# Kernel optimization log

Measured on AMD Instinct MI355X. Metric: run time of the kernel, lower is better.

## Reference

```python
import jax, jax.numpy as jnp
import numpy as np

B, N, C = 2, 2048, 768
H = 16
D = C // H  # head_dim = 48
SCALE = 1.0 / float(np.sqrt(D))


def setup_inputs() -> dict:
    key = jax.random.key(0)
    ks = jax.random.split(key, 5)
    x = jax.random.normal(ks[0], (B, N, C), dtype=jnp.float32)
    # torch nn.Linear weights are [out, in]; apply as x @ W.T
    qkv_w = jax.random.normal(ks[1], (3 * C, C), dtype=jnp.float32) * 0.02
    qkv_b = jax.random.normal(ks[2], (3 * C,), dtype=jnp.float32) * 0.02
    proj_w = jax.random.normal(ks[3], (C, C), dtype=jnp.float32) * 0.02
    proj_b = jax.random.normal(ks[4], (C,), dtype=jnp.float32) * 0.02
    return {"x": x, "qkv_w": qkv_w, "qkv_b": qkv_b, "proj_w": proj_w, "proj_b": proj_b}


def reference(x, qkv_w, qkv_b, proj_w, proj_b):
    # qkv: (B, N, 3C) -> (3, B, H, N, D)
    qkv = x @ qkv_w.T + qkv_b
    qkv = qkv.reshape(B, N, 3, H, D).transpose(2, 0, 3, 1, 4)
    q, k, v = qkv[0], qkv[1], qkv[2]
    # manual attention: full (B, H, N, N) score matrix, as in the original
    attn = jnp.einsum('bhqd,bhkd->bhqk', q, k) * SCALE
    attn = jax.nn.softmax(attn, axis=-1)
    # attn_drop with p=0.0 (eval / deterministic) is identity
    y = jnp.einsum('bhqk,bhkd->bhqd', attn, v)
    y = y.transpose(0, 2, 1, 3).reshape(B, N, C)
    return y @ proj_w.T + proj_b
```

## Files before the change

kernel.cpp:

```cpp
#include <hip/hip_runtime.h>

typedef short v8s __attribute__((ext_vector_type(8)));
typedef short v4s __attribute__((ext_vector_type(4)));
typedef float v4f __attribute__((ext_vector_type(4)));
typedef unsigned uint2v __attribute__((ext_vector_type(2)));
typedef unsigned uint4v __attribute__((ext_vector_type(4)));
typedef unsigned short u16;

#define NSEQ 2048
#define CDIM 768
#define NH   16
#define DH   48
#define DP   64
#define MROWS 4096
#define N3C  2304
#define BH   32

#if __has_builtin(__builtin_amdgcn_exp2f)
#define EXP2(x) __builtin_amdgcn_exp2f(x)
#else
#define EXP2(x) exp2f(x)
#endif
#if __has_builtin(__builtin_amdgcn_rcpf)
#define RCP(x) __builtin_amdgcn_rcpf(x)
#else
#define RCP(x) (1.0f/(x))
#endif

#if __has_builtin(__builtin_amdgcn_permlane32_swap) && __has_builtin(__builtin_amdgcn_permlane16_swap)
#define HAVE_PERMSWAP 1
#endif

__device__ __forceinline__ u16 f2bf(float f){
  unsigned u = __float_as_uint(f);
  u += 0x7FFFu + ((u>>16)&1u);
  return (u16)(u>>16);
}

#if __has_builtin(__builtin_amdgcn_cvt_pk_bf16_f32)
typedef __bf16 bf16x2_t __attribute__((ext_vector_type(2)));
__device__ __forceinline__ unsigned pkbf(float a, float b){
  bf16x2_t r = __builtin_amdgcn_cvt_pk_bf16_f32(a, b);
  return __builtin_bit_cast(unsigned, r);
}
#else
__device__ __forceinline__ unsigned pkbf(float a, float b){
  unsigned x = __float_as_uint(a), y = __float_as_uint(b);
  x += 0x7FFFu + ((x>>16)&1u);
  y += 0x7FFFu + ((y>>16)&1u);
  return (x>>16) | (y & 0xFFFF0000u);
}
#endif

__device__ __forceinline__ void load_lds16(const u16* g, u16* l){
  __builtin_amdgcn_global_load_lds((const __attribute__((address_space(1))) void*)g,
                                   (__attribute__((address_space(3))) void*)l, 16, 0, 0);
}

#define XN8  (MROWS*CDIM/8)
#define WN8  (N3C*CDIM/8)
#define PN8  (CDIM*CDIM/8)
#define CONVB ((XN8+WN8+PN8)/256)
__global__ __launch_bounds__(256) void prep(const float* __restrict__ x, const float* __restrict__ w,
                                            const float* __restrict__ pw, u16* __restrict__ dst,
                                            u16* __restrict__ q, u16* __restrict__ k){
  int bid = blockIdx.x;
  if (bid < CONVB){
    int i = bid*256 + threadIdx.x;
    const float* src;
    if (i < XN8)            src = x  + (size_t)i*8;
    else if (i < XN8+WN8)   src = w  + (size_t)(i - XN8)*8;
    else                    src = pw + (size_t)(i - XN8 - WN8)*8;
    v4f f0 = ((const v4f*)src)[0];
    v4f f1 = ((const v4f*)src)[1];
    v8s o;
#pragma unroll
    for (int j = 0; j < 4; j++) ((u16*)&o)[j]   = f2bf(f0[j]);
#pragma unroll
    for (int j = 0; j < 4; j++) ((u16*)&o)[4+j] = f2bf(f1[j]);
    ((v8s*)dst)[i] = o;
  } else {
    int idx = (bid - CONVB)*256 + threadIdx.x;
    v8s z = (v8s){0,0,0,0,0,0,0,0};
    int r = idx >> 1, half = idx & 1;
    *(v8s*)(q + (size_t)r*DP + DH + half*8) = z;
    *(v8s*)(k + (size_t)r*DP + DH + half*8) = z;
  }
}

__global__ __launch_bounds__(256) void qkv_gemm(const u16* __restrict__ x, const u16* __restrict__ w,
                                                const float* __restrict__ bias,
                                                u16* __restrict__ q, u16* __restrict__ k, u16* __restrict__ v){
  __shared__ __align__(16) u16 As[128*32];
  __shared__ __align__(16) u16 Bs[128*32];
  const int wave = threadIdx.x >> 6;
  const int lane = threadIdx.x & 63;
  const int l15  = lane & 15;
  const int quad = lane >> 4;
  const int wm = wave & 1, wn = wave >> 1;
  const int m0 = blockIdx.x*128, n0 = blockIdx.y*128;

  const int srow = lane >> 2;
  const int sg   = (lane & 3) ^ ((lane >> 3) & 3);
  const int sgoff = sg*8;

  v4f acc[4][4];
#pragma unroll
  for (int i = 0; i < 4; i++)
#pragma unroll
    for (int j = 0; j < 4; j++) acc[i][j] = (v4f){0.f,0.f,0.f,0.f};

  const int sig = (l15 >> 1) & 3;

  for (int kt = 0; kt < CDIM/32; kt++){
    const int k0 = kt*32;
    __syncthreads();
#pragma unroll
    for (int j = 0; j < 2; j++){
      int c = wave*2 + j;
      int r = c*16 + srow;
      load_lds16(x + (size_t)(m0 + r)*CDIM + k0 + sgoff, &As[c*512]);
      load_lds16(w + (size_t)(n0 + r)*CDIM + k0 + sgoff, &Bs[c*512]);
    }
    __syncthreads();

    v8s af[4], bf[4];
#pragma unroll
    for (int t = 0; t < 4; t++){
      int ra = wm*64 + t*16 + l15;
      af[t] = *(const v8s*)(&As[ra*32 + ((quad ^ sig)<<3)]);
      int rb = wn*64 + t*16 + l15;
      bf[t] = *(const v8s*)(&Bs[rb*32 + ((quad ^ sig)<<3)]);
    }
#pragma unroll
    for (int ti = 0; ti < 4; ti++)
#pragma unroll
      for (int tj = 0; tj < 4; tj++)
        acc[ti][tj] = __builtin_amdgcn_mfma_f32_16x16x32_bf16(af[ti], bf[tj], acc[ti][tj], 0, 0, 0);
  }

  const float QS = 0.2082540589f;
#pragma unroll
  for (int tj = 0; tj < 4; tj++){
    const int c = n0 + wn*64 + tj*16 + l15;
    const float bv = bias[c];
    const int t = c / CDIM;
    const int rem = c - t*CDIM;
    const int h = rem / DH;
    const int d = rem - h*DH;
#pragma unroll
    for (int ti = 0; ti < 4; ti++){
#pragma unroll
      for (int r = 0; r < 4; r++){
        int m = m0 + wm*64 + ti*16 + quad*4 + r;
        int b_ = m >> 11;
        int n  = m & (NSEQ-1);
        float val = acc[ti][tj][r] + bv;
        if (t == 0) val *= QS;
        u16 o  = f2bf(val);
        int bhn = b_*NH + h;
        if (t == 0)      q[((size_t)bhn*NSEQ + n)*DP + d] = o;
        else if (t == 1) k[((size_t)bhn*NSEQ + n)*DP + d] = o;
        else             v[((size_t)bhn*DP + d)*NSEQ + n] = o;
      }
    }
  }
}

__global__ __launch_bounds__(256, 4) void attn(const u16* __restrict__ q, const u16* __restrict__ k,
                                               const u16* __restrict__ v, u16* __restrict__ y){
  __shared__ __align__(16) u16 Kl[2][64*64];
  __shared__ __align__(16) u16 Vl[2][48*64];
#ifndef HAVE_PERMSWAP
  __shared__ __align__(16) u16 Pl[4*2*1024];
#endif
  const int bh = blockIdx.x;
  const int qt = blockIdx.y;
  const int wave = threadIdx.x >> 6;
  const int lane = threadIdx.x & 63;
  const int l15  = lane & 15;
  const int quad = lane >> 4;
  const int lo3  = l15 & 7;
  const u16* qb = q + (size_t)bh*NSEQ*DP;
  const u16* kb = k + (size_t)bh*NSEQ*DP;
  const u16* vb = v + (size_t)bh*DP*NSEQ;
  const int qm = qt*128 + wave*32;

  v8s qf[2][2];
#pragma unroll
  for (int si = 0; si < 2; si++)
#pragma unroll
    for (int ks = 0; ks < 2; ks++)
      qf[si][ks] = *(const v8s*)(qb + (size_t)(qm + si*16 + l15)*DP + ks*32 + quad*8);

  const short one = (short)0x3F80;
  const v8s vones = (l15 == 0) ? (v8s){one,one,one,one,one,one,one,one}
                               : (v8s){0,0,0,0,0,0,0,0};

  v4f o[2][4];
#pragma unroll
  for (int si = 0; si < 2; si++)
#pragma unroll
    for (int i = 0; i < 4; i++) o[si][i] = (v4f){0.f,0.f,0.f,0.f};

  const int sr  = lane >> 3;
  const int soff = ((lane & 7) ^ (sr & 7)) * 8;
#ifndef HAVE_PERMSWAP
  u16* Plw = Pl + wave*2048;
#endif

  const int krow0 = wave*8 + sr;
#define STAGE(kt_, b_) do{                                                              \
    load_lds16(kb + ((size_t)((kt_)*64 + krow0))*DP + soff,      &Kl[b_][krow0*64]);    \
    load_lds16(kb + ((size_t)((kt_)*64 + 32 + krow0))*DP + soff, &Kl[b_][(32+krow0)*64]);\
    load_lds16(vb + (size_t)krow0*NSEQ + (kt_)*64 + soff,        &Vl[b_][krow0*64]);    \
    if (wave < 2)                                                                       \
      load_lds16(vb + (size_t)(32+krow0)*NSEQ + (kt_)*64 + soff, &Vl[b_][(32+krow0)*64]);\
  } while(0)

  STAGE(0, 0);

  for (int i = 0; i < 32; i++){
    const int buf = i & 1;
    __syncthreads();
    if (i < 31) STAGE(i + 1, buf^1);

    const u16* Klb = &Kl[buf][0];
    const u16* Vlb = &Vl[buf][0];

    v4f s[2][4];
#pragma unroll
    for (int nt = 0; nt < 4; nt++){
      int rrow = nt*16 + l15;
      v8s kf0 = *(const v8s*)(&Klb[rrow*64 + ((quad ^ lo3)<<3)]);
      v8s kf1 = *(const v8s*)(&Klb[rrow*64 + (((4+quad) ^ lo3)<<3)]);
      s[0][nt] = __builtin_amdgcn_mfma_f32_16x16x32_bf16(kf0, qf[0][0], (v4f){0.f,0.f,0.f,0.f}, 0, 0, 0);
      s[0][nt] = __builtin_amdgcn_mfma_f32_16x16x32_bf16(kf1, qf[0][1], s[0][nt], 0, 0, 0);
      s[1][nt] = __builtin_amdgcn_mfma_f32_16x16x32_bf16(kf0, qf[1][0], (v4f){0.f,0.f,0.f,0.f}, 0, 0, 0);
      s[1][nt] = __builtin_amdgcn_mfma_f32_16x16x32_bf16(kf1, qf[1][1], s[1][nt], 0, 0, 0);
    }

    v8s pa[2][2];
#ifdef HAVE_PERMSWAP
#pragma unroll
    for (int si = 0; si < 2; si++){
      unsigned w[4][2];
#pragma unroll
      for (int nt = 0; nt < 4; nt++){
        w[nt][0] = pkbf(EXP2(s[si][nt][0]), EXP2(s[si][nt][1]));
        w[nt][1] = pkbf(EXP2(s[si][nt][2]), EXP2(s[si][nt][3]));
      }
#pragma unroll
      for (int ks = 0; ks < 2; ks++){
        unsigned W[4];
#pragma unroll
        for (int h = 0; h < 2; h++){
          auto a = __builtin_amdgcn_permlane32_swap(w[2*ks][h], w[2*ks+1][h], false, false);
          auto b = __builtin_amdgcn_permlane16_swap(a[0], a[1], false, false);
          W[h]   = b[0];
          W[2+h] = b[1];
        }
        uint4v u; u[0] = W[0]; u[1] = W[1]; u[2] = W[2]; u[3] = W[3];
        pa[si][ks] = __builtin_bit_cast(v8s, u);
      }
    }
#else
#pragma unroll
    for (int si = 0; si < 2; si++)
#pragma unroll
      for (int nt = 0; nt < 4; nt++){
        uint2v pw;
        pw.x = pkbf(EXP2(s[si][nt][0]), EXP2(s[si][nt][1]));
        pw.y = pkbf(EXP2(s[si][nt][2]), EXP2(s[si][nt][3]));
        int g = nt*2 + (quad>>1);
        *(uint2v*)(&Plw[si*1024 + l15*64 + ((g ^ lo3)<<3) + (quad&1)*4]) = pw;
      }
#pragma unroll
    for (int si = 0; si < 2; si++)
#pragma unroll
      for (int ks = 0; ks < 2; ks++){
        int ga = ks*4 + quad;
        pa[si][ks] = *(const v8s*)(&Plw[si*1024 + l15*64 + ((ga ^ lo3)<<3)]);
      }
#endif

#pragma unroll
    for (int dt = 0; dt < 3; dt++){
#pragma unroll
      for (int ks = 0; ks < 2; ks++){
        int row = dt*16 + l15;
        v8s vf = *(const v8s*)(&Vlb[row*64 + (((ks*4+quad) ^ lo3)<<3)]);
        o[0][dt] = __builtin_amdgcn_mfma_f32_16x16x32_bf16(pa[0][ks], vf, o[0][dt], 0, 0, 0);
        o[1][dt] = __builtin_amdgcn_mfma_f32_16x16x32_bf16(pa[1][ks], vf, o[1][dt], 0, 0, 0);
      }
    }
#pragma unroll
    for (int ks = 0; ks < 2; ks++){
      o[0][3] = __builtin_amdgcn_mfma_f32_16x16x32_bf16(pa[0][ks], vones, o[0][3], 0, 0, 0);
      o[1][3] = __builtin_amdgcn_mfma_f32_16x16x32_bf16(pa[1][ks], vones, o[1][3], 0, 0, 0);
    }
  }

  const int b_ = bh / NH, h = bh % NH;
#pragma unroll
  for (int si = 0; si < 2; si++){
#pragma unroll
    for (int r = 0; r < 4; r++){
      float l = __shfl(o[si][3][r], (lane & 48));
      float inv = RCP(l);
      int rowg = b_*NSEQ + qm + si*16 + quad*4 + r;
#pragma unroll
      for (int dt = 0; dt < 3; dt++)
        y[(size_t)rowg*CDIM + h*DH + dt*16 + l15] = f2bf(o[si][dt][r]*inv);
    }
  }
}

__global__ __launch_bounds__(256) void proj_gemm(const u16* __restrict__ y, const u16* __restrict__ w,
                                                 const float* __restrict__ bias, float* __restrict__ out){
  __shared__ __align__(16) u16 As[64*32];
  __shared__ __align__(16) u16 Bs[128*32];
  const int wave = threadIdx.x >> 6;
  const int lane = threadIdx.x & 63;
  const int l15  = lane & 15;
  const int quad = lane >> 4;
  const int wm = wave & 1, wn = wave >> 1;
  const int m0 = blockIdx.x*64, n0 = blockIdx.y*128;

  const int srow = lane >> 2;
  const int sg   = (lane & 3) ^ ((lane >> 3) & 3);
  const int sgoff = sg*8;

  v4f acc[2][4];
#pragma unroll
  for (int i = 0; i < 2; i++)
#pragma unroll
    for (int j = 0; j < 4; j++) acc[i][j] = (v4f){0.f,0.f,0.f,0.f};

  const int sig = (l15 >> 1) & 3;

  for (int kt = 0; kt < CDIM/32; kt++){
    const int k0 = kt*32;
    __syncthreads();
    {
      int rA = wave*16 + srow;
      load_lds16(y + (size_t)(m0 + rA)*CDIM + k0 + sgoff, &As[wave*512]);
#pragma unroll
      for (int j = 0; j < 2; j++){
        int c = wave*2 + j;
        int rB = c*16 + srow;
        load_lds16(w + (size_t)(n0 + rB)*CDIM + k0 + sgoff, &Bs[c*512]);
      }
    }
    __syncthreads();

    v8s af[2], bf[4];
#pragma unroll
    for (int t = 0; t < 2; t++){
      int ra = wm*32 + t*16 + l15;
      af[t] = *(const v8s*)(&As[ra*32 + ((quad ^ sig)<<3)]);
    }
#pragma unroll
    for (int t = 0; t < 4; t++){
      int rb = wn*64 + t*16 + l15;
      bf[t] = *(const v8s*)(&Bs[rb*32 + ((quad ^ sig)<<3)]);
    }
#pragma unroll
    for (int ti = 0; ti < 2; ti++)
#pragma unroll
      for (int tj = 0; tj < 4; tj++)
        acc[ti][tj] = __builtin_amdgcn_mfma_f32_16x16x32_bf16(af[ti], bf[tj], acc[ti][tj], 0, 0, 0);
  }

#pragma unroll
  for (int tj = 0; tj < 4; tj++){
    const int c = n0 + wn*64 + tj*16 + l15;
    const float bv = bias[c];
#pragma unroll
    for (int ti = 0; ti < 2; ti++){
#pragma unroll
      for (int r = 0; r < 4; r++){
        int m = m0 + wm*32 + ti*16 + quad*4 + r;
        out[(size_t)m*CDIM + c] = acc[ti][tj][r] + bv;
      }
    }
  }
}

extern "C" void kernel_launch(void* const* d_in, const int* in_sizes, int n_in,
                              void* d_out, int out_size, void* d_ws, size_t ws_size,
                              hipStream_t stream){
  const float* x      = (const float*)d_in[0];
  const float* qkv_w  = (const float*)d_in[1];
  const float* qkv_b  = (const float*)d_in[2];
  const float* proj_w = (const float*)d_in[3];
  const float* proj_b = (const float*)d_in[4];
  float* out = (float*)d_out;

  u16* xb  = (u16*)d_ws;
  u16* wb  = xb  + (size_t)MROWS*CDIM;
  u16* pwb = wb  + (size_t)N3C*CDIM;
  u16* q   = pwb + (size_t)CDIM*CDIM;
  u16* k   = q + (size_t)BH*NSEQ*DP;
  u16* v   = k + (size_t)BH*NSEQ*DP;
  u16* y = xb;

  prep<<<dim3(CONVB + 512), dim3(256), 0, stream>>>(x, qkv_w, proj_w, xb, q, k);
  qkv_gemm<<<dim3(MROWS/128, N3C/128), dim3(256), 0, stream>>>(xb, wb, qkv_b, q, k, v);
  attn<<<dim3(BH, NSEQ/128), dim3(256), 0, stream>>>(q, k, v, y);
  proj_gemm<<<dim3(MROWS/64, CDIM/128), dim3(256), 0, stream>>>(y, pwb, proj_b, out);
}
```

Measured before the change: 165.6 us.

## Triple-buffer K/V tiles in attention with explicit vmcnt waits

Moves the attention kernel's K/V LDS staging from double to triple buffering, prefetching two tiles ahead. A manual s_waitcnt vmcnt(3) plus s_barrier replaces __syncthreads so the async LDS loads for the next tile can stay in flight during compute. The goal is to hide global-load latency better. In exchange, LDS use per block rises, which may lower occupancy, and the hand-written wait count depends on how many loads each wave issues (waves 0-1 issue 4, others 3). The fallback path without permswap adds a __syncthreads inside the compute body.

```diff
diff --git a/kernel.cpp b/kernel.cpp
--- a/kernel.cpp
+++ b/kernel.cpp
@@ -169,8 +169,8 @@
 
 __global__ __launch_bounds__(256, 4) void attn(const u16* __restrict__ q, const u16* __restrict__ k,
                                                const u16* __restrict__ v, u16* __restrict__ y){
-  __shared__ __align__(16) u16 Kl[2][64*64];
-  __shared__ __align__(16) u16 Vl[2][48*64];
+  __shared__ __align__(16) u16 Kl[3][64*64];
+  __shared__ __align__(16) u16 Vl[3][48*64];
 #ifndef HAVE_PERMSWAP
   __shared__ __align__(16) u16 Pl[4*2*1024];
 #endif
@@ -186,23 +186,6 @@
   const u16* vb = v + (size_t)bh*DP*NSEQ;
   const int qm = qt*128 + wave*32;
 
-  v8s qf[2][2];
-#pragma unroll
-  for (int si = 0; si < 2; si++)
-#pragma unroll
-    for (int ks = 0; ks < 2; ks++)
-      qf[si][ks] = *(const v8s*)(qb + (size_t)(qm + si*16 + l15)*DP + ks*32 + quad*8);
-
-  const short one = (short)0x3F80;
-  const v8s vones = (l15 == 0) ? (v8s){one,one,one,one,one,one,one,one}
-                               : (v8s){0,0,0,0,0,0,0,0};
-
-  v4f o[2][4];
-#pragma unroll
-  for (int si = 0; si < 2; si++)
-#pragma unroll
-    for (int i = 0; i < 4; i++) o[si][i] = (v4f){0.f,0.f,0.f,0.f};
-
   const int sr  = lane >> 3;
   const int soff = ((lane & 7) ^ (sr & 7)) * 8;
 #ifndef HAVE_PERMSWAP
@@ -219,87 +202,114 @@
   } while(0)
 
   STAGE(0, 0);
-
-  for (int i = 0; i < 32; i++){
-    const int buf = i & 1;
-    __syncthreads();
-    if (i < 31) STAGE(i + 1, buf^1);
-
-    const u16* Klb = &Kl[buf][0];
-    const u16* Vlb = &Vl[buf][0];
-
-    v4f s[2][4];
-#pragma unroll
-    for (int nt = 0; nt < 4; nt++){
-      int rrow = nt*16 + l15;
-      v8s kf0 = *(const v8s*)(&Klb[rrow*64 + ((quad ^ lo3)<<3)]);
-      v8s kf1 = *(const v8s*)(&Klb[rrow*64 + (((4+quad) ^ lo3)<<3)]);
-      s[0][nt] = __builtin_amdgcn_mfma_f32_16x16x32_bf16(kf0, qf[0][0], (v4f){0.f,0.f,0.f,0.f}, 0, 0, 0);
-      s[0][nt] = __builtin_amdgcn_mfma_f32_16x16x32_bf16(kf1, qf[0][1], s[0][nt], 0, 0, 0);
-      s[1][nt] = __builtin_amdgcn_mfma_f32_16x16x32_bf16(kf0, qf[1][0], (v4f){0.f,0.f,0.f,0.f}, 0, 0, 0);
-      s[1][nt] = __builtin_amdgcn_mfma_f32_16x16x32_bf16(kf1, qf[1][1], s[1][nt], 0, 0, 0);
-    }
-
-    v8s pa[2][2];
+  STAGE(1, 1);
+
+  v8s qf[2][2];
+#pragma unroll
+  for (int si = 0; si < 2; si++)
+#pragma unroll
+    for (int ks = 0; ks < 2; ks++)
+      qf[si][ks] = *(const v8s*)(qb + (size_t)(qm + si*16 + l15)*DP + ks*32 + quad*8);
+
+  const short one = (short)0x3F80;
+  const v8s vones = (l15 == 0) ? (v8s){one,one,one,one,one,one,one,one}
+                               : (v8s){0,0,0,0,0,0,0,0};
+
+  v4f o[2][4];
+#pragma unroll
+  for (int si = 0; si < 2; si++)
+#pragma unroll
+    for (int i = 0; i < 4; i++) o[si][i] = (v4f){0.f,0.f,0.f,0.f};
+
+#define COMPUTE(sc_) do{                                                                          \
+    const u16* Klb = &Kl[sc_][0];                                                                 \
+    const u16* Vlb = &Vl[sc_][0];                                                                 \
+    v4f s[2][4];                                                                                  \
+    _Pragma("unroll")                                                                             \
+    for (int nt = 0; nt < 4; nt++){                                                               \
+      int rrow = nt*16 + l15;                                                                     \
+      v8s kf0 = *(const v8s*)(&Klb[rrow*64 + ((quad ^ lo3)<<3)]);                                 \
+      v8s kf1 = *(const v8s*)(&Klb[rrow*64 + (((4+quad) ^ lo3)<<3)]);                             \
+      s[0][nt] = __builtin_amdgcn_mfma_f32_16x16x32_bf16(kf0, qf[0][0], (v4f){0.f,0.f,0.f,0.f}, 0, 0, 0); \
+      s[0][nt] = __builtin_amdgcn_mfma_f32_16x16x32_bf16(kf1, qf[0][1], s[0][nt], 0, 0, 0);       \
+      s[1][nt] = __builtin_amdgcn_mfma_f32_16x16x32_bf16(kf0, qf[1][0], (v4f){0.f,0.f,0.f,0.f}, 0, 0, 0); \
+      s[1][nt] = __builtin_amdgcn_mfma_f32_16x16x32_bf16(kf1, qf[1][1], s[1][nt], 0, 0, 0);       \
+    }                                                                                             \
+    v8s pa[2][2];                                                                                 \
+    PTRANS                                                                                        \
+    _Pragma("unroll")                                                                             \
+    for (int dt = 0; dt < 3; dt++){                                                               \
+      _Pragma("unroll")                                                                           \
+      for (int ks = 0; ks < 2; ks++){                                                             \
+        int row = dt*16 + l15;                                                                    \
+        v8s vf = *(const v8s*)(&Vlb[row*64 + (((ks*4+quad) ^ lo3)<<3)]);                          \
+        o[0][dt] = __builtin_amdgcn_mfma_f32_16x16x32_bf16(pa[0][ks], vf, o[0][dt], 0, 0, 0);     \
+        o[1][dt] = __builtin_amdgcn_mfma_f32_16x16x32_bf16(pa[1][ks], vf, o[1][dt], 0, 0, 0);     \
+      }                                                                                           \
+    }                                                                                             \
+    _Pragma("unroll")                                                                             \
+    for (int ks = 0; ks < 2; ks++){                                                               \
+      o[0][3] = __builtin_amdgcn_mfma_f32_16x16x32_bf16(pa[0][ks], vones, o[0][3], 0, 0, 0);      \
+      o[1][3] = __builtin_amdgcn_mfma_f32_16x16x32_bf16(pa[1][ks], vones, o[1][3], 0, 0, 0);      \
+    }                                                                                             \
+  } while(0)
+
 #ifdef HAVE_PERMSWAP
-#pragma unroll
-    for (int si = 0; si < 2; si++){
-      unsigned w[4][2];
-#pragma unroll
-      for (int nt = 0; nt < 4; nt++){
-        w[nt][0] = pkbf(EXP2(s[si][nt][0]), EXP2(s[si][nt][1]));
-        w[nt][1] = pkbf(EXP2(s[si][nt][2]), EXP2(s[si][nt][3]));
+#define PTRANS                                                                                    \
+    _Pragma("unroll")                                                                             \
+    for (int si = 0; si < 2; si++){                                                               \
+      unsigned w[4][2];                                                                           \
+      _Pragma("unroll")                                                                           \
+      for (int nt = 0; nt < 4; nt++){                                                             \
+        w[nt][0] = pkbf(EXP2(s[si][nt][0]), EXP2(s[si][nt][1]));                                  \
+        w[nt][1] = pkbf(EXP2(s[si][nt][2]), EXP2(s[si][nt][3]));                                  \
+      }                                                                                           \
+      _Pragma("unroll")                                                                           \
+      for (int ks = 0; ks < 2; ks++){                                                             \
+        unsigned W[4];                                                                            \
+        _Pragma("unroll")                                                                         \
+        for (int h = 0; h < 2; h++){                                                              \
+          auto a = __builtin_amdgcn_permlane32_swap(w[2*ks][h], w[2*ks+1][h], false, false);      \
+          auto b = __builtin_amdgcn_permlane16_swap(a[0], a[1], false, false);                    \
+          W[h]   = b[0];                                                                          \
+          W[2+h] = b[1];                                                                          \
+        }                                                                                         \
+        uint4v u; u[0] = W[0]; u[1] = W[1]; u[2] = W[2]; u[3] = W[3];                             \
+        pa[si][ks] = __builtin_bit_cast(v8s, u);                                                  \
+      }                                                                                           \
+    }
+#else
+#define PTRANS                                                                                    \
+    _Pragma("unroll")                                                                             \
+    for (int si = 0; si < 2; si++)                                                                \
+      _Pragma("unroll")                                                                           \
+      for (int nt = 0; nt < 4; nt++){                                                             \
+        uint2v pw;                                                                                \
+        pw.x = pkbf(EXP2(s[si][nt][0]), EXP2(s[si][nt][1]));                                      \
+        pw.y = pkbf(EXP2(s[si][nt][2]), EXP2(s[si][nt][3]));                                      \
+        int g = nt*2 + (quad>>1);                                                                 \
+        *(uint2v*)(&Plw[si*1024 + l15*64 + ((g ^ lo3)<<3) + (quad&1)*4]) = pw;                    \
+      }                                                                                           \
+    __syncthreads();                                                                              \
+    _Pragma("unroll")                                                                             \
+    for (int si = 0; si < 2; si++)                                                                \
+      _Pragma("unroll")                                                                           \
+      for (int ks = 0; ks < 2; ks++){                                                             \
+        int ga = ks*4 + quad;                                                                     \
+        pa[si][ks] = *(const v8s*)(&Plw[si*1024 + l15*64 + ((ga ^ lo3)<<3)]);                     \
       }
-#pragma unroll
-      for (int ks = 0; ks < 2; ks++){
-        unsigned W[4];
-#pragma unroll
-        for (int h = 0; h < 2; h++){
-          auto a = __builtin_amdgcn_permlane32_swap(w[2*ks][h], w[2*ks+1][h], false, false);
-          auto b = __builtin_amdgcn_permlane16_swap(a[0], a[1], false, false);
-          W[h]   = b[0];
-          W[2+h] = b[1];
-        }
-        uint4v u; u[0] = W[0]; u[1] = W[1]; u[2] = W[2]; u[3] = W[3];
-        pa[si][ks] = __builtin_bit_cast(v8s, u);
-      }
-    }
-#else
-#pragma unroll
-    for (int si = 0; si < 2; si++)
-#pragma unroll
-      for (int nt = 0; nt < 4; nt++){
-        uint2v pw;
-        pw.x = pkbf(EXP2(s[si][nt][0]), EXP2(s[si][nt][1]));
-        pw.y = pkbf(EXP2(s[si][nt][2]), EXP2(s[si][nt][3]));
-        int g = nt*2 + (quad>>1);
-        *(uint2v*)(&Plw[si*1024 + l15*64 + ((g ^ lo3)<<3) + (quad&1)*4]) = pw;
-      }
-#pragma unroll
-    for (int si = 0; si < 2; si++)
-#pragma unroll
-      for (int ks = 0; ks < 2; ks++){
-        int ga = ks*4 + quad;
-        pa[si][ks] = *(const v8s*)(&Plw[si*1024 + l15*64 + ((ga ^ lo3)<<3)]);
-      }
-#endif
-
-#pragma unroll
-    for (int dt = 0; dt < 3; dt++){
-#pragma unroll
-      for (int ks = 0; ks < 2; ks++){
-        int row = dt*16 + l15;
-        v8s vf = *(const v8s*)(&Vlb[row*64 + (((ks*4+quad) ^ lo3)<<3)]);
-        o[0][dt] = __builtin_amdgcn_mfma_f32_16x16x32_bf16(pa[0][ks], vf, o[0][dt], 0, 0, 0);
-        o[1][dt] = __builtin_amdgcn_mfma_f32_16x16x32_bf16(pa[1][ks], vf, o[1][dt], 0, 0, 0);
-      }
-    }
-#pragma unroll
-    for (int ks = 0; ks < 2; ks++){
-      o[0][3] = __builtin_amdgcn_mfma_f32_16x16x32_bf16(pa[0][ks], vones, o[0][3], 0, 0, 0);
-      o[1][3] = __builtin_amdgcn_mfma_f32_16x16x32_bf16(pa[1][ks], vones, o[1][3], 0, 0, 0);
-    }
-  }
+#endif
+
+  int sc = 0, sw = 2;
+  for (int t = 0; t < 31; t++){
+    asm volatile("s_waitcnt vmcnt(3)\n\ts_barrier" ::: "memory");
+    if (t < 30) STAGE(t + 2, sw);
+    COMPUTE(sc);
+    sc = (sc == 2) ? 0 : sc + 1;
+    sw = (sw == 2) ? 0 : sw + 1;
+  }
+  asm volatile("s_waitcnt vmcnt(0)\n\ts_barrier" ::: "memory");
+  COMPUTE(sc);
 
   const int b_ = bh / NH, h = bh % NH;
 #pragma unroll
@@ -314,6 +324,9 @@
         y[(size_t)rowg*CDIM + h*DH + dt*16 + l15] = f2bf(o[si][dt][r]*inv);
     }
   }
+#undef STAGE
+#undef COMPUTE
+#undef PTRANS
 }
 
 __global__ __launch_bounds__(256) void proj_gemm(const u16* __restrict__ y, const u16* __restrict__ w,
```

Result: slower. 169.1 us (+2.1%).
